# Kernel tuning notes

Measured on AMD Instinct MI355X. Metric: run time of the kernel, lower is better.

Reference implementation:

```python
import jax, jax.numpy as jnp
import numpy as np

B, N, C = 16, 3136, 384
H = W = 56
HEADS = 8
DH = C // HEADS
AG = 49          # agent_num
PS = 7           # pool size (sqrt(agent_num)); H % PS == 0 -> exact block mean
OUT = 1000
SCALE = DH ** -0.5


def setup_inputs() -> dict:
    key = jax.random.key(0)
    ks = jax.random.split(key, 16)
    f32 = jnp.float32

    def nrm(k, sh, s=0.02):
        return jax.random.normal(k, sh, f32) * s

    return dict(
        x=jax.random.normal(ks[0], (B, N, C), f32),
        Wq=nrm(ks[1], (C, C)),
        Wkv=nrm(ks[2], (C, 2 * C)),
        an_bias=nrm(ks[3], (HEADS, AG, H, W)),
        na_bias=nrm(ks[4], (HEADS, AG, H, W)),
        ah_bias=nrm(ks[5], (1, HEADS, AG, H, 1)),
        aw_bias=nrm(ks[6], (1, HEADS, AG, 1, W)),
        ha_bias=nrm(ks[7], (1, HEADS, H, 1, AG)),
        wa_bias=nrm(ks[8], (1, HEADS, 1, W, AG)),
        dwc_w=nrm(ks[9], (C, 1, 3, 3), 0.1),   # depthwise 3x3, groups=C (OIHW, I=1)
        dwc_b=jnp.zeros((C,), f32),
        Wproj=nrm(ks[10], (C, C)),
        bproj=jnp.zeros((C,), f32),
        ln_g=jnp.ones((C,), f32),
        ln_b=jnp.zeros((C,), f32),
        W1=nrm(ks[11], (C, 2 * C)),
        b1=jnp.zeros((2 * C,), f32),
        W2=nrm(ks[12], (2 * C, OUT)),
        b2=jnp.zeros((OUT,), f32),
    )


def _layernorm(x, g, b, eps=1e-5):
    m = x.mean(-1, keepdims=True)
    v = ((x - m) ** 2).mean(-1, keepdims=True)
    return (x - m) * jax.lax.rsqrt(v + eps) * g + b


def reference(x, Wq, Wkv, an_bias, na_bias, ah_bias, aw_bias, ha_bias, wa_bias,
              dwc_w, dwc_b, Wproj, bproj, ln_g, ln_b, W1, b1, W2, b2):
    q = x @ Wq                                  # (B,N,C)
    kv = x @ Wkv                                # (B,N,2C)  (sr_ratio=1 path)
    k, v = kv[..., :C], kv[..., C:]

    # agent tokens: AdaptiveAvgPool2d(7) on (B,C,56,56) == exact 8x8 block mean
    agent = q.reshape(B, PS, H // PS, PS, W // PS, C).mean((2, 4)).reshape(B, AG, C)

    qh = q.reshape(B, N, HEADS, DH).transpose(0, 2, 1, 3)      # (B,h,N,d)
    kh = k.reshape(B, N, HEADS, DH).transpose(0, 2, 1, 3)
    vh = v.reshape(B, N, HEADS, DH).transpose(0, 2, 1, 3)
    ah = agent.reshape(B, AG, HEADS, DH).transpose(0, 2, 1, 3)  # (B,h,AG,d)

    # stage 1: agent -> kv. bilinear interp to same size == identity (sr=1)
    pos_bias = an_bias.reshape(1, HEADS, AG, N) + (ah_bias + aw_bias).reshape(1, HEADS, AG, N)
    agent_attn = jax.nn.softmax(
        jnp.einsum('bhad,bhnd->bhan', ah * SCALE, kh) + pos_bias, axis=-1)
    agent_v = jnp.einsum('bhan,bhnd->bhad', agent_attn, vh)     # (B,h,AG,d)

    # stage 2: query -> agent
    agent_bias = (na_bias.reshape(1, HEADS, AG, N).transpose(0, 1, 3, 2)
                  + (ha_bias + wa_bias).reshape(1, HEADS, N, AG))
    q_attn = jax.nn.softmax(
        jnp.einsum('bhnd,bhad->bhna', qh * SCALE, ah) + agent_bias, axis=-1)
    out = jnp.einsum('bhna,bhad->bhnd', q_attn, agent_v)
    out = out.transpose(0, 2, 1, 3).reshape(B, N, C)

    # depthwise conv residual on v (sr=1 -> no interpolation)
    v_img = v.reshape(B, H, W, C).transpose(0, 3, 1, 2)          # (B,C,H,W)
    dwc = jax.lax.conv_general_dilated(
        v_img, dwc_w, (1, 1), 'SAME', feature_group_count=C,
        dimension_numbers=('NCHW', 'OIHW', 'NCHW')) + dwc_b[None, :, None, None]
    out = out + dwc.transpose(0, 2, 3, 1).reshape(B, N, C)

    out = out @ Wproj + bproj
    pooled = out.mean(axis=1)                   # adaptive_avg_pool2d to 1x1
    h1 = _layernorm(pooled, ln_g, ln_b)
    h1 = jax.nn.gelu(h1 @ W1 + b1, approximate=False)
    return h1 @ W2 + b2                         # (B, OUT)
```

## Files before the change

### kernel.cpp

```cpp
#include <hip/hip_runtime.h>
#include <hip/hip_bf16.h>
#include <math.h>

#define BB 16
#define NN 3136
#define CC 384
#define HDS 8
#define DHH 48
#define AGG 49
#define HI 56
#define WI 56
#define OUTD 1000
#define SCALE_F 0.14433756729740643f
#define QKVC 1152

typedef __attribute__((ext_vector_type(8))) short short8;
typedef __attribute__((ext_vector_type(4))) float f32x4;

__device__ __forceinline__ float bf2f(unsigned short u) {
  union { unsigned u32; float f; } x;
  x.u32 = ((unsigned)u) << 16;
  return x.f;
}
__device__ __forceinline__ unsigned short f2bf(float f) {
  union { float f; unsigned u; } x;
  x.f = f;
  unsigned u = x.u;
  unsigned r = (u + 0x7fffu + ((u >> 16) & 1u)) >> 16;
  return (unsigned short)r;
}

__device__ __forceinline__ size_t xp_off(int gb, int ks, int j, int lane) {
  return ((((size_t)gb * 12 + ks) * 4 + j) * 64 + lane) * 8;
}
__device__ __forceinline__ size_t wp_off(int blk, int ks, int i, int lane) {
  return ((((size_t)blk * 12 + ks) * 4 + i) * 64 + lane) * 8;
}
__device__ __forceinline__ size_t vtp_off(int bh, int chunk, int half, int ntd, int lane) {
  return ((((size_t)bh * 49 + chunk) * 2 + half) * 3 + ntd) * 512 + lane * 8;
}

__global__ __launch_bounds__(256) void pack_x(const float* __restrict__ x,
                                              unsigned short* __restrict__ xp) {
  __shared__ unsigned short xlds[64 * 200];
  int gb = blockIdx.x;
  int tid = threadIdx.x;
  int lane = tid & 63, wv = tid >> 6;
  int lo = lane & 15, g = lane >> 4;
  int tok0 = gb * 64;

  for (int kh = 0; kh < 2; kh++) {
    if (kh) __syncthreads();
#pragma unroll
    for (int it = 0; it < 12; it++) {
      int idx = tid + it * 256;
      int tok = idx / 48, k4 = idx % 48;
      float4 f = *(const float4*)&x[(size_t)(tok0 + tok) * 384 + kh * 192 + k4 * 4];
      uint2 o;
      o.x = (unsigned)f2bf(f.x) | ((unsigned)f2bf(f.y) << 16);
      o.y = (unsigned)f2bf(f.z) | ((unsigned)f2bf(f.w) << 16);
      *(uint2*)&xlds[tok * 200 + k4 * 4] = o;
    }
    __syncthreads();
    for (int p = wv; p < 24; p += 4) {
      int ks = p >> 2, j = p & 3;
      uint4 v = *(const uint4*)&xlds[(j * 16 + lo) * 200 + ks * 32 + g * 8];
      *(uint4*)&xp[xp_off(gb, kh * 6 + ks, j, lane)] = v;
    }
  }
}

__global__ __launch_bounds__(256) void pack_w(const float* __restrict__ Wq,
                                              const float* __restrict__ Wkv,
                                              unsigned short* __restrict__ wp) {
  __shared__ unsigned short wlds[64 * 392];
  int blk = blockIdx.x;
  int col0 = blk * 64;
  const float* src;
  int ncol, nloc;
  if (col0 < 384) { src = Wq; ncol = 384; nloc = col0; }
  else            { src = Wkv; ncol = 768; nloc = col0 - 384; }
  int tid = threadIdx.x;
  int lane = tid & 63, wv = tid >> 6;
  int lo = lane & 15, g = lane >> 4;

#pragma unroll
  for (int it = 0; it < 96; it++) {
    int idx = tid + it * 256;
    int k = idx >> 6, col = idx & 63;
    wlds[col * 392 + k] = f2bf(src[(size_t)k * ncol + nloc + col]);
  }
  __syncthreads();
  for (int p = wv; p < 48; p += 4) {
    int ks = p >> 2, i = p & 3;
    uint4 v = *(const uint4*)&wlds[(i * 16 + lo) * 392 + ks * 32 + g * 8];
    *(uint4*)&wp[wp_off(blk, ks, i, lane)] = v;
  }
}

__global__ __launch_bounds__(256, 2) void gemm_v4(const unsigned short* __restrict__ xp,
// ... 40 lines not shown
  auto mfmaF = [&](short8* wf, short8* xf) {
    __builtin_amdgcn_s_setprio(1);
#pragma unroll
    for (int i = 0; i < 4; i++)
#pragma unroll
      for (int jj = 0; jj < 8; jj++)
        acc[i][jj] = __builtin_amdgcn_mfma_f32_16x16x32_bf16(wf[i], xf[jj], acc[i][jj], 0, 0, 0);
    __builtin_amdgcn_s_setprio(0);
  };

  loadF(wfA, xfA, 0);
#pragma unroll
  for (int kp = 0; kp < 6; kp++) {
    loadF(wfB, xfB, 2 * kp + 1);
    mfmaF(wfA, xfA);
    if (kp < 5) loadF(wfA, xfA, 2 * kp + 2);
    mfmaF(wfB, xfB);
  }

#pragma unroll
  for (int jj = 0; jj < 8; jj++) {
    int token = (gbb + (jj >> 2)) * 64 + (jj & 3) * 16 + lo;
#pragma unroll
    for (int i = 0; i < 4; i++) {
      int ncol = bx * 128 + wn2 * 64 + i * 16 + g * 4;
      uint2 o;
      o.x = (unsigned)f2bf(acc[i][jj][0]) | ((unsigned)f2bf(acc[i][jj][1]) << 16);
      o.y = (unsigned)f2bf(acc[i][jj][2]) | ((unsigned)f2bf(acc[i][jj][3]) << 16);
      *(uint2*)&Y[(size_t)token * QKVC + ncol] = o;
    }
  }
}

__global__ __launch_bounds__(256) void make_cbias2(
    const float* __restrict__ na, const float* __restrict__ ha,
    const float* __restrict__ wa, const float* __restrict__ an,
    const float* __restrict__ ah, const float* __restrict__ aw,
    unsigned short* __restrict__ cb1t, unsigned short* __restrict__ cb2t) {
  int blk = blockIdx.x;
  int h = blk / 49, nc = blk % 49;
  int a = threadIdx.x & 63, sub = threadIdx.x >> 6;
  int ac = a < AGG ? a : AGG - 1;
  bool va = a < AGG;
  size_t hab = (size_t)h * AGG + ac;
#pragma unroll
  for (int i = 0; i < 16; i++) {
    int n = nc * 64 + i * 4 + sub;
    int r = n / WI, c = n % WI;
    float v1 = na[hab * NN + n] + ha[(h * HI + r) * AGG + ac] + wa[(h * WI + c) * AGG + ac];
    float v2 = an[hab * NN + n] + ah[hab * HI + r] + aw[hab * WI + c];
    size_t ob = ((size_t)h * NN + n) * 52;
    if (a < 52) {
      cb1t[ob + a] = va ? f2bf(v1) : (unsigned short)0;
      cb2t[ob + a] = va ? f2bf(v2) : (unsigned short)0;
    }
  }
}

#define VSTR 396
__global__ __launch_bounds__(256) void pack_vt(const unsigned short* __restrict__ qkv,
                                               unsigned short* __restrict__ vtp) {
  __shared__ unsigned short vlds[64 * VSTR];
  int blk = blockIdx.x;
  int b = blk / 49, chunk = blk % 49;
  int tid = threadIdx.x, lane = tid & 63, wv = tid >> 6;
  int lo = lane & 15, g = lane >> 4;

#pragma unroll
  for (int it = 0; it < 12; it++) {
    int idx = tid + it * 256;
    int t = idx / 48, d8 = idx % 48;
    short8 v = *(const short8*)&qkv[((size_t)b * NN + chunk * 64 + t) * QKVC + 768 + d8 * 8];
    *(uint2*)&vlds[t * VSTR + d8 * 8] = ((uint2*)&v)[0];
    *(uint2*)&vlds[t * VSTR + d8 * 8 + 4] = ((uint2*)&v)[1];
  }
  __syncthreads();
  int bh8 = b * 8;
#pragma unroll
  for (int p = 0; p < 12; p++) {
    int fid = wv * 12 + p;
    int h = fid / 6, rem = fid % 6, half = rem / 3, ntd = rem % 3;
    unsigned short tmp[8];
#pragma unroll
    for (int e = 0; e < 8; e++)
      tmp[e] = vlds[(half * 32 + g * 8 + e) * VSTR + h * 48 + ntd * 16 + lo];
    *(uint4*)&vtp[vtp_off(bh8 + h, chunk, half, ntd, lane)] = *(uint4*)tmp;
  }
}

__global__ __launch_bounds__(384) void pool_agent(const unsigned short* __restrict__ qkv,
                                                  unsigned short* __restrict__ agbf) {
  int blk = blockIdx.x;
  int b = blk / AGG, a = blk % AGG;
  int p1 = a / 7, p2 = a % 7;
  int c = threadIdx.x;
  float s = 0.f;
#pragma unroll
  for (int i = 0; i < 8; i++)
#pragma unroll
    for (int j = 0; j < 8; j++) {
      int n = (p1 * 8 + i) * WI + (p2 * 8 + j);
      s += bf2f(qkv[((size_t)b * NN + n) * QKVC + c]);
    }
  agbf[(size_t)blk * CC + c] = f2bf(s * (1.f / 64.f));
}

__global__ __launch_bounds__(256) void agent_attn_v5(
    const unsigned short* __restrict__ qkv, const unsigned short* __restrict__ agbf,
    const unsigned short* __restrict__ cb2t, const unsigned short* __restrict__ vtp,
    float* __restrict__ lpart, float* __restrict__ avpart) {
  int z = blockIdx.x;
  int s = z & 3;
  int h = (z >> 2) & 7;
  int b = z >> 5;
  int tid = threadIdx.x, lane = tid & 63, wv = tid >> 6;
  int lo = lane & 15, g = lane >> 4;
  int slot = s * 4 + wv;
  int cstart = (slot == 0) ? 0 : 3 * slot + 1;
  int ccount = (slot == 0) ? 4 : 3;
  int bh = b * 8 + h;

  __shared__ __align__(16) unsigned short pT[4][64 * 72];
  __shared__ float ldsAV[AGG * 48];
  __shared__ float ldsL[AGG];
  for (int i = tid; i < AGG * 48; i += 256) ldsAV[i] = 0.f;
  if (tid < AGG) ldsL[tid] = 0.f;
  __syncthreads();

  short8 af0[4], af1[4];
#pragma unroll
  for (int mt = 0; mt < 4; mt++) {
    int a = mt * 16 + lo;
    int ac = a < AGG ? a : AGG - 1;
    const unsigned short* p = agbf + ((size_t)b * AGG + ac) * CC + h * 48;
    af0[mt] = *(const short8*)(p + g * 8);
    if (g < 2) af1[mt] = *(const short8*)(p + 32 + g * 8);
    else { short8 zz = {0, 0, 0, 0, 0, 0, 0, 0}; af1[mt] = zz; }
  }

  f32x4 acc2[4][3];
#pragma unroll
  for (int mt = 0; mt < 4; mt++)
#pragma unroll
    for (int ntd = 0; ntd < 3; ntd++) acc2[mt][ntd] = (f32x4)0.f;
  float lacc[4][4];
#pragma unroll
  for (int mt = 0; mt < 4; mt++)
#pragma unroll
    for (int r = 0; r < 4; r++) lacc[mt][r] = 0.f;

  for (int ci = 0; ci < ccount; ci++) {
    int chunk = cstart + ci;
    int nb = chunk * 64;

    short8 kf0[4], kf1[4];
#pragma unroll
    for (int nt = 0; nt < 4; nt++) {
      const unsigned short* kp = qkv + ((size_t)b * NN + nb + nt * 16 + lo) * QKVC + 384 + h * 48;
      kf0[nt] = *(const short8*)(kp + g * 8);
      if (g < 2) kf1[nt] = *(const short8*)(kp + 32 + g * 8);
      else { short8 zz = {0, 0, 0, 0, 0, 0, 0, 0}; kf1[nt] = zz; }
    }
    ushort4 cbv[4][4];
#pragma unroll
    for (int mt = 0; mt < 4; mt++)
#pragma unroll
      for (int nt = 0; nt < 4; nt++)
        cbv[mt][nt] = *(const ushort4*)&cb2t[((size_t)h * NN + nb + nt * 16 + lo) * 52 + mt * 16 + g * 4];
    short8 vb0[3], vb1[3];
#pragma unroll
    for (int ntd = 0; ntd < 3; ntd++) {
      vb0[ntd] = *(const short8*)&vtp[vtp_off(bh, chunk, 0, ntd, lane)];
      vb1[ntd] = *(const short8*)&vtp[vtp_off(bh, chunk, 1, ntd, lane)];
    }

    f32x4 acc[4][4];
#pragma unroll
    for (int mt = 0; mt < 4; mt++)
#pragma unroll
      for (int nt = 0; nt < 4; nt++) acc[mt][nt] = (f32x4)0.f;
#pragma unroll
    for (int mt = 0; mt < 4; mt++)
#pragma unroll
      for (int nt = 0; nt < 4; nt++) {
        acc[mt][nt] = __builtin_amdgcn_mfma_f32_16x16x32_bf16(af0[mt], kf0[nt], acc[mt][nt], 0, 0, 0);
        acc[mt][nt] = __builtin_amdgcn_mfma_f32_16x16x32_bf16(af1[mt], kf1[nt], acc[mt][nt], 0, 0, 0);
      }

#pragma unroll
    for (int mt = 0; mt < 4; mt++)
#pragma unroll
      for (int nt = 0; nt < 4; nt++) {
        unsigned short cb4[4] = {cbv[mt][nt].x, cbv[mt][nt].y, cbv[mt][nt].z, cbv[mt][nt].w};
#pragma unroll
        for (int r = 0; r < 4; r++) {
          int a = mt * 16 + g * 4 + r;
          float e = 0.f;
          if (a < AGG) e = __expf(acc[mt][nt][r] * SCALE_F + bf2f(cb4[r]));
          acc[mt][nt][r] = e;
        }
      }
#pragma unroll
    for (int mt = 0; mt < 4; mt++)
#pragma unroll
      for (int r = 0; r < 4; r++)
        lacc[mt][r] += acc[mt][0][r] + acc[mt][1][r] + acc[mt][2][r] + acc[mt][3][r];
#pragma unroll
    for (int mt = 0; mt < 4; mt++)
#pragma unroll
      for (int nt = 0; nt < 4; nt++)
#pragma unroll
        for (int r = 0; r < 4; r++) {
          int a = mt * 16 + g * 4 + r;
          int t = nt * 16 + lo;
          pT[wv][a * 72 + t] = f2bf(acc[mt][nt][r]);
        }

    short8 pa0[4], pa1[4];
#pragma unroll
    for (int mt = 0; mt < 4; mt++) {
      const unsigned short* p = &pT[wv][(mt * 16 + lo) * 72 + g * 8];
      pa0[mt] = *(const short8*)p;
      pa1[mt] = *(const short8*)(p + 32);
    }
#pragma unroll
    for (int mt = 0; mt < 4; mt++)
#pragma unroll
      for (int ntd = 0; ntd < 3; ntd++) {
        acc2[mt][ntd] = __builtin_amdgcn_mfma_f32_16x16x32_bf16(pa0[mt], vb0[ntd], acc2[mt][ntd], 0, 0, 0);
        acc2[mt][ntd] = __builtin_amdgcn_mfma_f32_16x16x32_bf16(pa1[mt], vb1[ntd], acc2[mt][ntd], 0, 0, 0);
      }
  }

#pragma unroll
  for (int mt = 0; mt < 4; mt++)
#pragma unroll
    for (int r = 0; r < 4; r++) {
      float v = lacc[mt][r];
      v += __shfl_xor(v, 1); v += __shfl_xor(v, 2);
      v += __shfl_xor(v, 4); v += __shfl_xor(v, 8);
      if (lo == 0) {
        int a = mt * 16 + g * 4 + r;
        if (a < AGG) atomicAdd(&ldsL[a], v);
      }
    }
#pragma unroll
  for (int mt = 0; mt < 4; mt++)
#pragma unroll
    for (int ntd = 0; ntd < 3; ntd++)
#pragma unroll
      for (int r = 0; r < 4; r++) {
        int a = mt * 16 + g * 4 + r;
        if (a < AGG) atomicAdd(&ldsAV[a * 48 + ntd * 16 + lo], acc2[mt][ntd][r]);
      }
  __syncthreads();
  size_t pbase = (size_t)bh * 4 + s;
  for (int i = tid; i < AGG * 48; i += 256) avpart[pbase * 2352 + i] = ldsAV[i];
  if (tid < AGG) lpart[pbase * AGG + tid] = ldsL[tid];
}

__global__ __launch_bounds__(256) void av_normalize4(const float* __restrict__ lpart,
                                                     const float* __restrict__ avpart,
                                                     float* __restrict__ av) {
  int bh = blockIdx.x;
  int tid = threadIdx.x;
  __shared__ float linv[AGG];
  if (tid < AGG) {
    float l = 0.f;
#pragma unroll
    for (int s = 0; s < 4; s++) l += lpart[((size_t)bh * 4 + s) * AGG + tid];
    linv[tid] = 1.f / l;
  }
  __syncthreads();
  for (int idx = tid; idx < AGG * 48; idx += 256) {
    int a = idx / 48;
    float v = 0.f;
#pragma unroll
    for (int s = 0; s < 4; s++) v += avpart[((size_t)bh * 4 + s) * 2352 + idx];
    av[(size_t)bh * 2352 + idx] = v * linv[a];
  }
}

__global__ __launch_bounds__(256) void q_attn_v9(
    const unsigned short* __restrict__ qkv, const unsigned short* __restrict__ agbf,
    const unsigned short* __restrict__ cb1t, float* __restrict__ opart) {
  int z = blockIdx.x;
  int s = z & 3;
  int h = (z >> 2) & 7;
  int b = z >> 5;
  int tid = threadIdx.x, lane = tid & 63, wv = tid >> 6;
  int lo = lane & 15, g = lane >> 4;
  int slot = s * 4 + wv;
  int cstart = (slot == 0) ? 0 : 3 * slot + 1;
  int ccount = (slot == 0) ? 4 : 3;
  int bh = b * 8 + h;

  short8 af0[4], af1[4];
#pragma unroll
  for (int mt = 0; mt < 4; mt++) {
    int a = mt * 16 + lo;
    int ac = a < AGG ? a : AGG - 1;
    const unsigned short* p = agbf + ((size_t)b * AGG + ac) * CC + h * 48;
    af0[mt] = *(const short8*)(p + g * 8);
    if (g < 2) af1[mt] = *(const short8*)(p + 32 + g * 8);
    else { short8 zz = {0, 0, 0, 0, 0, 0, 0, 0}; af1[mt] = zz; }
  }

  float psum[4][4];
#pragma unroll
  for (int mt = 0; mt < 4; mt++)
#pragma unroll
    for (int r = 0; r < 4; r++) psum[mt][r] = 0.f;

  for (int ci = 0; ci < ccount; ci++) {
    int nb = (cstart + ci) * 64;

    short8 qf0[4], qf1[4];
#pragma unroll
    for (int nt = 0; nt < 4; nt++) {
      const unsigned short* qp = qkv + ((size_t)b * NN + nb + nt * 16 + lo) * QKVC + h * 48;
      qf0[nt] = *(const short8*)(qp + g * 8);
      if (g < 2) qf1[nt] = *(const short8*)(qp + 32 + g * 8);
      else { short8 zz = {0, 0, 0, 0, 0, 0, 0, 0}; qf1[nt] = zz; }
    }
    ushort4 cbv[4][4];
#pragma unroll
    for (int mt = 0; mt < 4; mt++)
#pragma unroll
      for (int nt = 0; nt < 4; nt++)
        cbv[mt][nt] = *(const ushort4*)&cb1t[((size_t)h * NN + nb + nt * 16 + lo) * 52 + mt * 16 + g * 4];

    f32x4 acc[4][4];
#pragma unroll
    for (int mt = 0; mt < 4; mt++)
#pragma unroll
      for (int nt = 0; nt < 4; nt++) acc[mt][nt] = (f32x4)0.f;
#pragma unroll
    for (int mt = 0; mt < 4; mt++)
#pragma unroll
      for (int nt = 0; nt < 4; nt++) {
        acc[mt][nt] = __builtin_amdgcn_mfma_f32_16x16x32_bf16(af0[mt], qf0[nt], acc[mt][nt], 0, 0, 0);
        acc[mt][nt] = __builtin_amdgcn_mfma_f32_16x16x32_bf16(af1[mt], qf1[nt], acc[mt][nt], 0, 0, 0);
      }

#pragma unroll
    for (int nt = 0; nt < 4; nt++) {
      float lsum = 0.f;
#pragma unroll
      for (int mt = 0; mt < 4; mt++) {
        unsigned short cb4[4] = {cbv[mt][nt].x, cbv[mt][nt].y, cbv[mt][nt].z, cbv[mt][nt].w};
#pragma unroll
        for (int r = 0; r < 4; r++) {
          int a = mt * 16 + g * 4 + r;
          float e = 0.f;
          if (a < AGG) e = __expf(acc[mt][nt][r] * SCALE_F + bf2f(cb4[r]));
          acc[mt][nt][r] = e;
          lsum += e;
        }
      }
      lsum += __shfl_xor(lsum, 16);
      lsum += __shfl_xor(lsum, 32);
      float inv = 1.f / lsum;
#pragma unroll
      for (int mt = 0; mt < 4; mt++)
#pragma unroll
        for (int r = 0; r < 4; r++)
          psum[mt][r] += acc[mt][nt][r] * inv;
    }
  }

  size_t pbase = (size_t)bh * 16 + slot;
#pragma unroll
  for (int mt = 0; mt < 4; mt++)
#pragma unroll
    for (int r = 0; r < 4; r++) {
      float v = psum[mt][r];
      v += __shfl_xor(v, 1); v += __shfl_xor(v, 2);
      v += __shfl_xor(v, 4); v += __shfl_xor(v, 8);
      int a = mt * 16 + g * 4 + r;
      if (lo == 0 && a < AGG) opart[pbase * 52 + a] = v;
    }
}

__global__ __launch_bounds__(384) void dwc_rows(const unsigned short* __restrict__ qkv,
                                                float* __restrict__ rowsum,
                                                float* __restrict__ edge0,
                                                float* __restrict__ edge1) {
  int z = blockIdx.x;
  int b = z / HI, r = z % HI;
  int c = threadIdx.x;
  const unsigned short* base = qkv + ((size_t)b * NN + (size_t)r * WI) * QKVC + 768 + c;
  float s = 0.f, e0 = 0.f, e1 = 0.f;
  for (int w = 0; w < WI; w++) {
    float v = bf2f(base[(size_t)w * QKVC]);
    s += v;
    if (w == 0) e0 = v;
    if (w == WI - 1) e1 = v;
  }
  rowsum[(size_t)z * CC + c] = s;
  edge0[(size_t)z * CC + c] = e0;
  edge1[(size_t)z * CC + c] = e1;
}

__global__ __launch_bounds__(384) void dwc_combine1(const float* __restrict__ rowsum,
                                                    const float* __restrict__ edge0,
                                                    const float* __restrict__ edge1,
                                                    float* __restrict__ dpart,
                                                    float* __restrict__ dedge) {
  int z = blockIdx.x;
  int b = z / 7, rc = z % 7;
  int c = threadIdx.x;
  float T = 0.f, C0 = 0.f, C55 = 0.f;
#pragma unroll
  for (int rr = 0; rr < 8; rr++) {
    int r = rc * 8 + rr;
    size_t idx = ((size_t)(b * HI + r)) * CC + c;
    float rs = rowsum[idx], a0 = edge0[idx], a1 = edge1[idx];
    T += rs; C0 += a0; C55 += a1;
    if (r == 0) {
      dedge[((size_t)b * 6 + 0) * CC + c] = rs;
      dedge[((size_t)b * 6 + 1) * CC + c] = a0;
      dedge[((size_t)b * 6 + 2) * CC + c] = a1;
    }
    if (r == HI - 1) {
      dedge[((size_t)b * 6 + 3) * CC + c] = rs;
      dedge[((size_t)b * 6 + 4) * CC + c] = a0;
      dedge[((size_t)b * 6 + 5) * CC + c] = a1;
    }
  }
  size_t pb = ((size_t)(b * 7 + rc) * 3) * CC + c;
  dpart[pb] = T;
  dpart[pb + CC] = C0;
  dpart[pb + 2 * CC] = C55;
}
// ... 196 lines not shown
  const float* W1 = (const float*)d_in[15];
  const float* b1 = (const float*)d_in[16];
  const float* W2 = (const float*)d_in[17];
  const float* b2 = (const float*)d_in[18];
  float* out = (float*)d_out;

  const size_t M = (size_t)BB * NN;
  char* wsp = (char*)d_ws;
  unsigned short* xp = (unsigned short*)wsp;
  unsigned short* vtp = xp;
  wsp += M * CC * 2;
  unsigned short* wpb = (unsigned short*)wsp;   wsp += (size_t)QKVC * CC * 2;
  unsigned short* qkv = (unsigned short*)wsp;   wsp += M * QKVC * 2;
  unsigned short* agbf = (unsigned short*)wsp;  wsp += (size_t)784 * CC * 2;
  unsigned short* cb1t = (unsigned short*)wsp;  wsp += (size_t)HDS * NN * 52 * 2;
  unsigned short* cb2t = (unsigned short*)wsp;  wsp += (size_t)HDS * NN * 52 * 2;
  float* lpart = (float*)wsp;                   wsp += (size_t)128 * 4 * AGG * 4;
  float* avpart = (float*)wsp;                  wsp += (size_t)128 * 4 * 2352 * 4;
  float* av = (float*)wsp;                      wsp += (size_t)128 * 2352 * 4;
  float* opart = (float*)wsp;                   wsp += (size_t)128 * 16 * 52 * 4;
  float* rowsum = (float*)wsp;                  wsp += (size_t)BB * HI * CC * 4;
  float* edge0 = (float*)wsp;                   wsp += (size_t)BB * HI * CC * 4;
  float* edge1 = (float*)wsp;                   wsp += (size_t)BB * HI * CC * 4;
  float* dpart = (float*)wsp;                   wsp += (size_t)BB * 7 * 3 * CC * 4;
  float* dedge = (float*)wsp;                   wsp += (size_t)BB * 6 * CC * 4;
  float* pre = (float*)wsp;                     wsp += (size_t)BB * CC * 4;
  float* pjpart = (float*)wsp;                  wsp += (size_t)BB * 6 * CC * 4;
  float* h0b = (float*)wsp;                     wsp += (size_t)BB * CC * 4;
  float* h1part = (float*)wsp;                  wsp += (size_t)BB * 6 * 2 * CC * 4;
  float* h1b = (float*)wsp;                     wsp += (size_t)BB * 2 * CC * 4;
  float* o2part = (float*)wsp;                  wsp += (size_t)BB * 12 * 1024 * 4;

  dim3 blk256(256);
  hipLaunchKernelGGL(pack_x, dim3(784), blk256, 0, stream, x, xp);
  hipLaunchKernelGGL(pack_w, dim3(18), blk256, 0, stream, Wq, Wkv, wpb);
  hipLaunchKernelGGL(make_cbias2, dim3(HDS * 49), blk256, 0, stream, na_bias,
                     ha_bias, wa_bias, an_bias, ah_bias, aw_bias, cb1t, cb2t);
  hipLaunchKernelGGL(gemm_v4, dim3(1764), blk256, 0, stream, xp, wpb, qkv);
  hipLaunchKernelGGL(pack_vt, dim3(BB * 49), blk256, 0, stream, qkv, vtp);
  hipLaunchKernelGGL(pool_agent, dim3(BB * AGG), dim3(384), 0, stream, qkv, agbf);
  hipLaunchKernelGGL(agent_attn_v5, dim3(BB * HDS * 4), blk256, 0, stream,
                     qkv, agbf, cb2t, vtp, lpart, avpart);
  hipLaunchKernelGGL(av_normalize4, dim3(BB * HDS), blk256, 0, stream, lpart,
                     avpart, av);
  hipLaunchKernelGGL(q_attn_v9, dim3(BB * HDS * 4), blk256, 0, stream, qkv,
                     agbf, cb1t, opart);
  hipLaunchKernelGGL(dwc_rows, dim3(BB * HI), dim3(384), 0, stream, qkv, rowsum,
                     edge0, edge1);
  hipLaunchKernelGGL(dwc_combine1, dim3(BB * 7), dim3(384), 0, stream, rowsum,
                     edge0, edge1, dpart, dedge);
  hipLaunchKernelGGL(head_pre, dim3(BB), dim3(384), 0, stream, dpart, dedge,
                     opart, av, dwc_w, dwc_b, pre);
  hipLaunchKernelGGL(head_proj_part, dim3(144), blk256, 0, stream, pre, Wproj, pjpart);
  hipLaunchKernelGGL(head_ln6, dim3(BB), dim3(384), 0, stream, pjpart, bproj,
                     ln_g, ln_b, h0b);
  hipLaunchKernelGGL(head_mlp1_part, dim3(288), blk256, 0, stream, h0b, W1, h1part);
  hipLaunchKernelGGL(head_mlp1_red, dim3(BB), blk256, 0, stream, h1part, b1, h1b);
  hipLaunchKernelGGL(head_mlp2_part, dim3(768), blk256, 0, stream, h1b, W2, o2part);
  hipLaunchKernelGGL(head_out, dim3(BB), blk256, 0, stream, o2part, b2, out);
}
```

Measured before the change: 265.8 us.

## Merge independent kernels into block-indexed fused launches to cut launch count

Combines independent kernels into shared launches that branch on block index. pack_x runs with make_cbias2, pack_vt with pool_agent, and agent attention with query attention and the dwc row sums. This removes several launch gaps and lets independent work fill the GPU together. In exchange, the fused kernels share the largest LDS footprint and register pressure of their branches, which may lower occupancy for the lighter blocks. pool_agent and dwc_rows now run at 256 threads looping over channels instead of 384.

```diff
diff --git a/kernel.cpp b/kernel.cpp
--- a/kernel.cpp
+++ b/kernel.cpp
@@ -40,32 +40,57 @@
   return ((((size_t)bh * 49 + chunk) * 2 + half) * 3 + ntd) * 512 + lane * 8;
 }
 
-__global__ __launch_bounds__(256) void pack_x(const float* __restrict__ x,
-                                              unsigned short* __restrict__ xp) {
+__global__ __launch_bounds__(256) void pack_x_cbias(
+    const float* __restrict__ x, unsigned short* __restrict__ xp,
+    const float* __restrict__ na, const float* __restrict__ ha,
+    const float* __restrict__ wa, const float* __restrict__ an,
+    const float* __restrict__ ah, const float* __restrict__ aw,
+    unsigned short* __restrict__ cb1t, unsigned short* __restrict__ cb2t) {
   __shared__ unsigned short xlds[64 * 200];
-  int gb = blockIdx.x;
+  int z = blockIdx.x;
   int tid = threadIdx.x;
-  int lane = tid & 63, wv = tid >> 6;
-  int lo = lane & 15, g = lane >> 4;
-  int tok0 = gb * 64;
-
-  for (int kh = 0; kh < 2; kh++) {
-    if (kh) __syncthreads();
-#pragma unroll
-    for (int it = 0; it < 12; it++) {
-      int idx = tid + it * 256;
-      int tok = idx / 48, k4 = idx % 48;
-      float4 f = *(const float4*)&x[(size_t)(tok0 + tok) * 384 + kh * 192 + k4 * 4];
-      uint2 o;
-      o.x = (unsigned)f2bf(f.x) | ((unsigned)f2bf(f.y) << 16);
-      o.y = (unsigned)f2bf(f.z) | ((unsigned)f2bf(f.w) << 16);
-      *(uint2*)&xlds[tok * 200 + k4 * 4] = o;
-    }
-    __syncthreads();
-    for (int p = wv; p < 24; p += 4) {
-      int ks = p >> 2, j = p & 3;
-      uint4 v = *(const uint4*)&xlds[(j * 16 + lo) * 200 + ks * 32 + g * 8];
-      *(uint4*)&xp[xp_off(gb, kh * 6 + ks, j, lane)] = v;
+  if (z < 784) {
+    int gb = z;
+    int lane = tid & 63, wv = tid >> 6;
+    int lo = lane & 15, g = lane >> 4;
+    int tok0 = gb * 64;
+    for (int kh = 0; kh < 2; kh++) {
+      if (kh) __syncthreads();
+#pragma unroll
+      for (int it = 0; it < 12; it++) {
+        int idx = tid + it * 256;
+        int tok = idx / 48, k4 = idx % 48;
+        float4 f = *(const float4*)&x[(size_t)(tok0 + tok) * 384 + kh * 192 + k4 * 4];
+        uint2 o;
+        o.x = (unsigned)f2bf(f.x) | ((unsigned)f2bf(f.y) << 16);
+        o.y = (unsigned)f2bf(f.z) | ((unsigned)f2bf(f.w) << 16);
+        *(uint2*)&xlds[tok * 200 + k4 * 4] = o;
+      }
+      __syncthreads();
+      for (int p = wv; p < 24; p += 4) {
+        int ks = p >> 2, j = p & 3;
+        uint4 v = *(const uint4*)&xlds[(j * 16 + lo) * 200 + ks * 32 + g * 8];
+        *(uint4*)&xp[xp_off(gb, kh * 6 + ks, j, lane)] = v;
+      }
+    }
+  } else {
+    int blk = z - 784;
+    int h = blk / 49, nc = blk % 49;
+    int a = tid & 63, sub = tid >> 6;
+    int ac = a < AGG ? a : AGG - 1;
+    bool va = a < AGG;
+    size_t hab = (size_t)h * AGG + ac;
+#pragma unroll
+    for (int i = 0; i < 16; i++) {
+      int n = nc * 64 + i * 4 + sub;
+      int r = n / WI, c = n % WI;
+      float v1 = na[hab * NN + n] + ha[(h * HI + r) * AGG + ac] + wa[(h * WI + c) * AGG + ac];
+      float v2 = an[hab * NN + n] + ah[hab * HI + r] + aw[hab * WI + c];
+      size_t ob = ((size_t)h * NN + n) * 52;
+      if (a < 52) {
+        cb1t[ob + a] = va ? f2bf(v1) : (unsigned short)0;
+        cb2t[ob + a] = va ? f2bf(v2) : (unsigned short)0;
+      }
     }
   }
 }
@@ -172,231 +197,327 @@
   }
 }
 
-__global__ __launch_bounds__(256) void make_cbias2(
-    const float* __restrict__ na, const float* __restrict__ ha,
-    const float* __restrict__ wa, const float* __restrict__ an,
-    const float* __restrict__ ah, const float* __restrict__ aw,
-    unsigned short* __restrict__ cb1t, unsigned short* __restrict__ cb2t) {
-  int blk = blockIdx.x;
-  int h = blk / 49, nc = blk % 49;
-  int a = threadIdx.x & 63, sub = threadIdx.x >> 6;
-  int ac = a < AGG ? a : AGG - 1;
-  bool va = a < AGG;
-  size_t hab = (size_t)h * AGG + ac;
-#pragma unroll
-  for (int i = 0; i < 16; i++) {
-    int n = nc * 64 + i * 4 + sub;
-    int r = n / WI, c = n % WI;
-    float v1 = na[hab * NN + n] + ha[(h * HI + r) * AGG + ac] + wa[(h * WI + c) * AGG + ac];
-    float v2 = an[hab * NN + n] + ah[hab * HI + r] + aw[hab * WI + c];
-    size_t ob = ((size_t)h * NN + n) * 52;
-    if (a < 52) {
-      cb1t[ob + a] = va ? f2bf(v1) : (unsigned short)0;
-      cb2t[ob + a] = va ? f2bf(v2) : (unsigned short)0;
-    }
-  }
-}
-
 #define VSTR 396
-__global__ __launch_bounds__(256) void pack_vt(const unsigned short* __restrict__ qkv,
-                                               unsigned short* __restrict__ vtp) {
+__global__ __launch_bounds__(256) void prep2_fused(const unsigned short* __restrict__ qkv,
+                                                   unsigned short* __restrict__ vtp,
+                                                   unsigned short* __restrict__ agbf) {
   __shared__ unsigned short vlds[64 * VSTR];
-  int blk = blockIdx.x;
-  int b = blk / 49, chunk = blk % 49;
-  int tid = threadIdx.x, lane = tid & 63, wv = tid >> 6;
-  int lo = lane & 15, g = lane >> 4;
-
-#pragma unroll
-  for (int it = 0; it < 12; it++) {
-    int idx = tid + it * 256;
-    int t = idx / 48, d8 = idx % 48;
-    short8 v = *(const short8*)&qkv[((size_t)b * NN + chunk * 64 + t) * QKVC + 768 + d8 * 8];
-    *(uint2*)&vlds[t * VSTR + d8 * 8] = ((uint2*)&v)[0];
-    *(uint2*)&vlds[t * VSTR + d8 * 8 + 4] = ((uint2*)&v)[1];
-  }
-  __syncthreads();
-  int bh8 = b * 8;
-#pragma unroll
-  for (int p = 0; p < 12; p++) {
-    int fid = wv * 12 + p;
-    int h = fid / 6, rem = fid % 6, half = rem / 3, ntd = rem % 3;
-    unsigned short tmp[8];
-#pragma unroll
-    for (int e = 0; e < 8; e++)
-      tmp[e] = vlds[(half * 32 + g * 8 + e) * VSTR + h * 48 + ntd * 16 + lo];
-    *(uint4*)&vtp[vtp_off(bh8 + h, chunk, half, ntd, lane)] = *(uint4*)tmp;
-  }
-}
-
-__global__ __launch_bounds__(384) void pool_agent(const unsigned short* __restrict__ qkv,
-                                                  unsigned short* __restrict__ agbf) {
-  int blk = blockIdx.x;
-  int b = blk / AGG, a = blk % AGG;
-  int p1 = a / 7, p2 = a % 7;
-  int c = threadIdx.x;
-  float s = 0.f;
-#pragma unroll
-  for (int i = 0; i < 8; i++)
-#pragma unroll
-    for (int j = 0; j < 8; j++) {
-      int n = (p1 * 8 + i) * WI + (p2 * 8 + j);
-      s += bf2f(qkv[((size_t)b * NN + n) * QKVC + c]);
-    }
-  agbf[(size_t)blk * CC + c] = f2bf(s * (1.f / 64.f));
-}
-
-__global__ __launch_bounds__(256) void agent_attn_v5(
+  int z = blockIdx.x;
+  int tid = threadIdx.x;
+  if (z < 784) {
+    int b = z / 49, chunk = z % 49;
+    int lane = tid & 63, wv = tid >> 6;
+    int lo = lane & 15, g = lane >> 4;
+#pragma unroll
+    for (int it = 0; it < 12; it++) {
+      int idx = tid + it * 256;
+      int t = idx / 48, d8 = idx % 48;
+      short8 v = *(const short8*)&qkv[((size_t)b * NN + chunk * 64 + t) * QKVC + 768 + d8 * 8];
+      *(uint2*)&vlds[t * VSTR + d8 * 8] = ((uint2*)&v)[0];
+      *(uint2*)&vlds[t * VSTR + d8 * 8 + 4] = ((uint2*)&v)[1];
+    }
+    __syncthreads();
+    int bh8 = b * 8;
+#pragma unroll
+    for (int p = 0; p < 12; p++) {
+      int fid = wv * 12 + p;
+      int h = fid / 6, rem = fid % 6, half = rem / 3, ntd = rem % 3;
+      unsigned short tmp[8];
+#pragma unroll
+      for (int e = 0; e < 8; e++)
+        tmp[e] = vlds[(half * 32 + g * 8 + e) * VSTR + h * 48 + ntd * 16 + lo];
+      *(uint4*)&vtp[vtp_off(bh8 + h, chunk, half, ntd, lane)] = *(uint4*)tmp;
+    }
+  } else {
+    int blk = z - 784;
+    int b = blk / AGG, a = blk % AGG;
+    int p1 = a / 7, p2 = a % 7;
+    for (int c = tid; c < CC; c += 256) {
+      float s = 0.f;
+#pragma unroll
+      for (int i = 0; i < 8; i++)
+#pragma unroll
+        for (int j = 0; j < 8; j++) {
+          int n = (p1 * 8 + i) * WI + (p2 * 8 + j);
+          s += bf2f(qkv[((size_t)b * NN + n) * QKVC + c]);
+        }
+      agbf[(size_t)blk * CC + c] = f2bf(s * (1.f / 64.f));
+    }
+  }
+}
+
+__global__ __launch_bounds__(256) void attn_dwc_fused(
     const unsigned short* __restrict__ qkv, const unsigned short* __restrict__ agbf,
-    const unsigned short* __restrict__ cb2t, const unsigned short* __restrict__ vtp,
-    float* __restrict__ lpart, float* __restrict__ avpart) {
-  int z = blockIdx.x;
-  int s = z & 3;
-  int h = (z >> 2) & 7;
-  int b = z >> 5;
-  int tid = threadIdx.x, lane = tid & 63, wv = tid >> 6;
-  int lo = lane & 15, g = lane >> 4;
-  int slot = s * 4 + wv;
-  int cstart = (slot == 0) ? 0 : 3 * slot + 1;
-  int ccount = (slot == 0) ? 4 : 3;
-  int bh = b * 8 + h;
-
+    const unsigned short* __restrict__ cb1t, const unsigned short* __restrict__ cb2t,
+    const unsigned short* __restrict__ vtp, float* __restrict__ lpart,
+    float* __restrict__ avpart, float* __restrict__ opart,
+    float* __restrict__ rowsum, float* __restrict__ edge0,
+    float* __restrict__ edge1) {
   __shared__ __align__(16) unsigned short pT[4][64 * 72];
   __shared__ float ldsAV[AGG * 48];
   __shared__ float ldsL[AGG];
-  for (int i = tid; i < AGG * 48; i += 256) ldsAV[i] = 0.f;
-  if (tid < AGG) ldsL[tid] = 0.f;
-  __syncthreads();
-
-  short8 af0[4], af1[4];
-#pragma unroll
-  for (int mt = 0; mt < 4; mt++) {
-    int a = mt * 16 + lo;
-    int ac = a < AGG ? a : AGG - 1;
-    const unsigned short* p = agbf + ((size_t)b * AGG + ac) * CC + h * 48;
-    af0[mt] = *(const short8*)(p + g * 8);
-    if (g < 2) af1[mt] = *(const short8*)(p + 32 + g * 8);
-    else { short8 zz = {0, 0, 0, 0, 0, 0, 0, 0}; af1[mt] = zz; }
-  }
-
-  f32x4 acc2[4][3];
-#pragma unroll
-  for (int mt = 0; mt < 4; mt++)
-#pragma unroll
-    for (int ntd = 0; ntd < 3; ntd++) acc2[mt][ntd] = (f32x4)0.f;
-  float lacc[4][4];
-#pragma unroll
-  for (int mt = 0; mt < 4; mt++)
-#pragma unroll
-    for (int r = 0; r < 4; r++) lacc[mt][r] = 0.f;
-
-  for (int ci = 0; ci < ccount; ci++) {
-    int chunk = cstart + ci;
-    int nb = chunk * 64;
-
-    short8 kf0[4], kf1[4];
-#pragma unroll
-    for (int nt = 0; nt < 4; nt++) {
-      const unsigned short* kp = qkv + ((size_t)b * NN + nb + nt * 16 + lo) * QKVC + 384 + h * 48;
-      kf0[nt] = *(const short8*)(kp + g * 8);
-      if (g < 2) kf1[nt] = *(const short8*)(kp + 32 + g * 8);
-      else { short8 zz = {0, 0, 0, 0, 0, 0, 0, 0}; kf1[nt] = zz; }
-    }
-    ushort4 cbv[4][4];
+
+  int z = blockIdx.x;
+  int tid = threadIdx.x, lane = tid & 63, wv = tid >> 6;
+  int lo = lane & 15, g = lane >> 4;
+
+  if (z < 512) {
+    int s = z & 3;
+    int h = (z >> 2) & 7;
+    int b = z >> 5;
+    int slot = s * 4 + wv;
+    int cstart = (slot == 0) ? 0 : 3 * slot + 1;
+    int ccount = (slot == 0) ? 4 : 3;
+    int bh = b * 8 + h;
+
+    for (int i = tid; i < AGG * 48; i += 256) ldsAV[i] = 0.f;
+    if (tid < AGG) ldsL[tid] = 0.f;
+    __syncthreads();
+
+    short8 af0[4], af1[4];
+#pragma unroll
+    for (int mt = 0; mt < 4; mt++) {
+      int a = mt * 16 + lo;
+      int ac = a < AGG ? a : AGG - 1;
+      const unsigned short* p = agbf + ((size_t)b * AGG + ac) * CC + h * 48;
+      af0[mt] = *(const short8*)(p + g * 8);
+      if (g < 2) af1[mt] = *(const short8*)(p + 32 + g * 8);
+      else { short8 zz = {0, 0, 0, 0, 0, 0, 0, 0}; af1[mt] = zz; }
+    }
+
+    f32x4 acc2[4][3];
 #pragma unroll
     for (int mt = 0; mt < 4; mt++)
 #pragma unroll
-      for (int nt = 0; nt < 4; nt++)
-        cbv[mt][nt] = *(const ushort4*)&cb2t[((size_t)h * NN + nb + nt * 16 + lo) * 52 + mt * 16 + g * 4];
-    short8 vb0[3], vb1[3];
-#pragma unroll
-    for (int ntd = 0; ntd < 3; ntd++) {
-      vb0[ntd] = *(const short8*)&vtp[vtp_off(bh, chunk, 0, ntd, lane)];
-      vb1[ntd] = *(const short8*)&vtp[vtp_off(bh, chunk, 1, ntd, lane)];
-    }
-
-    f32x4 acc[4][4];
+      for (int ntd = 0; ntd < 3; ntd++) acc2[mt][ntd] = (f32x4)0.f;
+    float lacc[4][4];
 #pragma unroll
     for (int mt = 0; mt < 4; mt++)
 #pragma unroll
-      for (int nt = 0; nt < 4; nt++) acc[mt][nt] = (f32x4)0.f;
+      for (int r = 0; r < 4; r++) lacc[mt][r] = 0.f;
+
+    for (int ci = 0; ci < ccount; ci++) {
+      int chunk = cstart + ci;
+      int nb = chunk * 64;
+
+      short8 kf0[4], kf1[4];
+#pragma unroll
+      for (int nt = 0; nt < 4; nt++) {
+        const unsigned short* kp = qkv + ((size_t)b * NN + nb + nt * 16 + lo) * QKVC + 384 + h * 48;
+        kf0[nt] = *(const short8*)(kp + g * 8);
+        if (g < 2) kf1[nt] = *(const short8*)(kp + 32 + g * 8);
+        else { short8 zz = {0, 0, 0, 0, 0, 0, 0, 0}; kf1[nt] = zz; }
+      }
+      ushort4 cbv[4][4];
+#pragma unroll
+      for (int mt = 0; mt < 4; mt++)
+#pragma unroll
+        for (int nt = 0; nt < 4; nt++)
+          cbv[mt][nt] = *(const ushort4*)&cb2t[((size_t)h * NN + nb + nt * 16 + lo) * 52 + mt * 16 + g * 4];
+      short8 vb0[3], vb1[3];
+#pragma unroll
+      for (int ntd = 0; ntd < 3; ntd++) {
+        vb0[ntd] = *(const short8*)&vtp[vtp_off(bh, chunk, 0, ntd, lane)];
+        vb1[ntd] = *(const short8*)&vtp[vtp_off(bh, chunk, 1, ntd, lane)];
+      }
+
+      f32x4 acc[4][4];
+#pragma unroll
+      for (int mt = 0; mt < 4; mt++)
+#pragma unroll
+        for (int nt = 0; nt < 4; nt++) acc[mt][nt] = (f32x4)0.f;
+#pragma unroll
+      for (int mt = 0; mt < 4; mt++)
+#pragma unroll
+        for (int nt = 0; nt < 4; nt++) {
+          acc[mt][nt] = __builtin_amdgcn_mfma_f32_16x16x32_bf16(af0[mt], kf0[nt], acc[mt][nt], 0, 0, 0);
+          acc[mt][nt] = __builtin_amdgcn_mfma_f32_16x16x32_bf16(af1[mt], kf1[nt], acc[mt][nt], 0, 0, 0);
+        }
+
+#pragma unroll
+      for (int mt = 0; mt < 4; mt++)
+#pragma unroll
+        for (int nt = 0; nt < 4; nt++) {
+          unsigned short cb4[4] = {cbv[mt][nt].x, cbv[mt][nt].y, cbv[mt][nt].z, cbv[mt][nt].w};
+#pragma unroll
+          for (int r = 0; r < 4; r++) {
+            int a = mt * 16 + g * 4 + r;
+            float e = 0.f;
+            if (a < AGG) e = __expf(acc[mt][nt][r] * SCALE_F + bf2f(cb4[r]));
+            acc[mt][nt][r] = e;
+          }
+        }
+#pragma unroll
+      for (int mt = 0; mt < 4; mt++)
+#pragma unroll
+        for (int r = 0; r < 4; r++)
+          lacc[mt][r] += acc[mt][0][r] + acc[mt][1][r] + acc[mt][2][r] + acc[mt][3][r];
+#pragma unroll
+      for (int mt = 0; mt < 4; mt++)
+#pragma unroll
+        for (int nt = 0; nt < 4; nt++)
+#pragma unroll
+          for (int r = 0; r < 4; r++) {
+            int a = mt * 16 + g * 4 + r;
+            int t = nt * 16 + lo;
+            pT[wv][a * 72 + t] = f2bf(acc[mt][nt][r]);
+          }
+
+      short8 pa0[4], pa1[4];
+#pragma unroll
+      for (int mt = 0; mt < 4; mt++) {
+        const unsigned short* p = &pT[wv][(mt * 16 + lo) * 72 + g * 8];
+        pa0[mt] = *(const short8*)p;
+        pa1[mt] = *(const short8*)(p + 32);
+      }
+#pragma unroll
+      for (int mt = 0; mt < 4; mt++)
+#pragma unroll
+        for (int ntd = 0; ntd < 3; ntd++) {
+          acc2[mt][ntd] = __builtin_amdgcn_mfma_f32_16x16x32_bf16(pa0[mt], vb0[ntd], acc2[mt][ntd], 0, 0, 0);
+          acc2[mt][ntd] = __builtin_amdgcn_mfma_f32_16x16x32_bf16(pa1[mt], vb1[ntd], acc2[mt][ntd], 0, 0, 0);
+        }
+    }
+
 #pragma unroll
     for (int mt = 0; mt < 4; mt++)
 #pragma unroll
-      for (int nt = 0; nt < 4; nt++) {
-        acc[mt][nt] = __builtin_amdgcn_mfma_f32_16x16x32_bf16(af0[mt], kf0[nt], acc[mt][nt], 0, 0, 0);
-        acc[mt][nt] = __builtin_amdgcn_mfma_f32_16x16x32_bf16(af1[mt], kf1[nt], acc[mt][nt], 0, 0, 0);
-      }
-
+      for (int r = 0; r < 4; r++) {
+        float v = lacc[mt][r];
+        v += __shfl_xor(v, 1); v += __shfl_xor(v, 2);
+        v += __shfl_xor(v, 4); v += __shfl_xor(v, 8);
+        if (lo == 0) {
+          int a = mt * 16 + g * 4 + r;
+          if (a < AGG) atomicAdd(&ldsL[a], v);
+        }
+      }
 #pragma unroll
     for (int mt = 0; mt < 4; mt++)
 #pragma unroll
-      for (int nt = 0; nt < 4; nt++) {
-        unsigned short cb4[4] = {cbv[mt][nt].x, cbv[mt][nt].y, cbv[mt][nt].z, cbv[mt][nt].w};
+      for (int ntd = 0; ntd < 3; ntd++)
 #pragma unroll
         for (int r = 0; r < 4; r++) {
           int a = mt * 16 + g * 4 + r;
-          float e = 0.f;
-          if (a < AGG) e = __expf(acc[mt][nt][r] * SCALE_F + bf2f(cb4[r]));
-          acc[mt][nt][r] = e;
+          if (a < AGG) atomicAdd(&ldsAV[a * 48 + ntd * 16 + lo], acc2[mt][ntd][r]);
         }
-      }
+    __syncthreads();
+    size_t pbase = (size_t)bh * 4 + s;
+    for (int i = tid; i < AGG * 48; i += 256) avpart[pbase * 2352 + i] = ldsAV[i];
+    if (tid < AGG) lpart[pbase * AGG + tid] = ldsL[tid];
+
+  } else if (z < 1024) {
+    int zz = z - 512;
+    int s = zz & 3;
+    int h = (zz >> 2) & 7;
+    int b = zz >> 5;
+    int slot = s * 4 + wv;
+    int cstart = (slot == 0) ? 0 : 3 * slot + 1;
+    int ccount = (slot == 0) ? 4 : 3;
+    int bh = b * 8 + h;
+
+    short8 af0[4], af1[4];
+#pragma unroll
+    for (int mt = 0; mt < 4; mt++) {
+      int a = mt * 16 + lo;
+      int ac = a < AGG ? a : AGG - 1;
+      const unsigned short* p = agbf + ((size_t)b * AGG + ac) * CC + h * 48;
+      af0[mt] = *(const short8*)(p + g * 8);
+      if (g < 2) af1[mt] = *(const short8*)(p + 32 + g * 8);
+      else { short8 zz2 = {0, 0, 0, 0, 0, 0, 0, 0}; af1[mt] = zz2; }
+    }
+
+    float psum[4][4];
 #pragma unroll
     for (int mt = 0; mt < 4; mt++)
 #pragma unroll
-      for (int r = 0; r < 4; r++)
-        lacc[mt][r] += acc[mt][0][r] + acc[mt][1][r] + acc[mt][2][r] + acc[mt][3][r];
+      for (int r = 0; r < 4; r++) psum[mt][r] = 0.f;
+
+    for (int ci = 0; ci < ccount; ci++) {
+      int nb = (cstart + ci) * 64;
+
+      short8 qf0[4], qf1[4];
+#pragma unroll
+      for (int nt = 0; nt < 4; nt++) {
+        const unsigned short* qp = qkv + ((size_t)b * NN + nb + nt * 16 + lo) * QKVC + h * 48;
+        qf0[nt] = *(const short8*)(qp + g * 8);
+        if (g < 2) qf1[nt] = *(const short8*)(qp + 32 + g * 8);
+        else { short8 zz2 = {0, 0, 0, 0, 0, 0, 0, 0}; qf1[nt] = zz2; }
+      }
+      ushort4 cbv[4][4];
+#pragma unroll
+      for (int mt = 0; mt < 4; mt++)
+#pragma unroll
+        for (int nt = 0; nt < 4; nt++)
+          cbv[mt][nt] = *(const ushort4*)&cb1t[((size_t)h * NN + nb + nt * 16 + lo) * 52 + mt * 16 + g * 4];
+
+      f32x4 acc[4][4];
+#pragma unroll
+      for (int mt = 0; mt < 4; mt++)
+#pragma unroll
+        for (int nt = 0; nt < 4; nt++) acc[mt][nt] = (f32x4)0.f;
+#pragma unroll
+      for (int mt = 0; mt < 4; mt++)
+#pragma unroll
+        for (int nt = 0; nt < 4; nt++) {
+          acc[mt][nt] = __builtin_amdgcn_mfma_f32_16x16x32_bf16(af0[mt], qf0[nt], acc[mt][nt], 0, 0, 0);
+          acc[mt][nt] = __builtin_amdgcn_mfma_f32_16x16x32_bf16(af1[mt], qf1[nt], acc[mt][nt], 0, 0, 0);
+        }
+
+#pragma unroll
+      for (int nt = 0; nt < 4; nt++) {
+        float lsum = 0.f;
+#pragma unroll
+        for (int mt = 0; mt < 4; mt++) {
+          unsigned short cb4[4] = {cbv[mt][nt].x, cbv[mt][nt].y, cbv[mt][nt].z, cbv[mt][nt].w};
+#pragma unroll
+          for (int r = 0; r < 4; r++) {
+            int a = mt * 16 + g * 4 + r;
+            float e = 0.f;
+            if (a < AGG) e = __expf(acc[mt][nt][r] * SCALE_F + bf2f(cb4[r]));
+            acc[mt][nt][r] = e;
+            lsum += e;
+          }
+        }
+        lsum += __shfl_xor(lsum, 16);
+        lsum += __shfl_xor(lsum, 32);
+        float inv = 1.f / lsum;
+#pragma unroll
+        for (int mt = 0; mt < 4; mt++)
+#pragma unroll
+          for (int r = 0; r < 4; r++)
+            psum[mt][r] += acc[mt][nt][r] * inv;
+      }
+    }
+
+    size_t pbase = (size_t)bh * 16 + slot;
 #pragma unroll
     for (int mt = 0; mt < 4; mt++)
 #pragma unroll
-      for (int nt = 0; nt < 4; nt++)
-#pragma unroll
-        for (int r = 0; r < 4; r++) {
-          int a = mt * 16 + g * 4 + r;
-          int t = nt * 16 + lo;
-          pT[wv][a * 72 + t] = f2bf(acc[mt][nt][r]);
-        }
-
-    short8 pa0[4], pa1[4];
-#pragma unroll
-    for (int mt = 0; mt < 4; mt++) {
-      const unsigned short* p = &pT[wv][(mt * 16 + lo) * 72 + g * 8];
-      pa0[mt] = *(const short8*)p;
-      pa1[mt] = *(const short8*)(p + 32);
-    }
-#pragma unroll
-    for (int mt = 0; mt < 4; mt++)
-#pragma unroll
-      for (int ntd = 0; ntd < 3; ntd++) {
-        acc2[mt][ntd] = __builtin_amdgcn_mfma_f32_16x16x32_bf16(pa0[mt], vb0[ntd], acc2[mt][ntd], 0, 0, 0);
-        acc2[mt][ntd] = __builtin_amdgcn_mfma_f32_16x16x32_bf16(pa1[mt], vb1[ntd], acc2[mt][ntd], 0, 0, 0);
-      }
-  }
-
-#pragma unroll
-  for (int mt = 0; mt < 4; mt++)
-#pragma unroll
-    for (int r = 0; r < 4; r++) {
-      float v = lacc[mt][r];
-      v += __shfl_xor(v, 1); v += __shfl_xor(v, 2);
-      v += __shfl_xor(v, 4); v += __shfl_xor(v, 8);
-      if (lo == 0) {
+      for (int r = 0; r < 4; r++) {
+        float v = psum[mt][r];
+        v += __shfl_xor(v, 1); v += __shfl_xor(v, 2);
+        v += __shfl_xor(v, 4); v += __shfl_xor(v, 8);
         int a = mt * 16 + g * 4 + r;
-        if (a < AGG) atomicAdd(&ldsL[a], v);
-      }
-    }
-#pragma unroll
-  for (int mt = 0; mt < 4; mt++)
-#pragma unroll
-    for (int ntd = 0; ntd < 3; ntd++)
-#pragma unroll
-      for (int r = 0; r < 4; r++) {
-        int a = mt * 16 + g * 4 + r;
-        if (a < AGG) atomicAdd(&ldsAV[a * 48 + ntd * 16 + lo], acc2[mt][ntd][r]);
-      }
-  __syncthreads();
-  size_t pbase = (size_t)bh * 4 + s;
-  for (int i = tid; i < AGG * 48; i += 256) avpart[pbase * 2352 + i] = ldsAV[i];
-  if (tid < AGG) lpart[pbase * AGG + tid] = ldsL[tid];
+        if (lo == 0 && a < AGG) opart[pbase * 52 + a] = v;
+      }
+
+  } else {
+    int zz = z - 1024;
+    int b = zz / HI, r = zz % HI;
+    for (int c = tid; c < CC; c += 256) {
+      const unsigned short* base = qkv + ((size_t)b * NN + (size_t)r * WI) * QKVC + 768 + c;
+      float sum = 0.f, e0v = 0.f, e1v = 0.f;
+      for (int w = 0; w < WI; w++) {
+        float v = bf2f(base[(size_t)w * QKVC]);
+        sum += v;
+        if (w == 0) e0v = v;
+        if (w == WI - 1) e1v = v;
+      }
+      rowsum[(size_t)zz * CC + c] = sum;
+      edge0[(size_t)zz * CC + c] = e0v;
+      edge1[(size_t)zz * CC + c] = e1v;
+    }
+  }
 }
 
 __global__ __launch_bounds__(256) void av_normalize4(const float* __restrict__ lpart,
@@ -419,127 +540,6 @@
     for (int s = 0; s < 4; s++) v += avpart[((size_t)bh * 4 + s) * 2352 + idx];
     av[(size_t)bh * 2352 + idx] = v * linv[a];
   }
-}
-
-__global__ __launch_bounds__(256) void q_attn_v9(
-    const unsigned short* __restrict__ qkv, const unsigned short* __restrict__ agbf,
-    const unsigned short* __restrict__ cb1t, float* __restrict__ opart) {
-  int z = blockIdx.x;
-  int s = z & 3;
-  int h = (z >> 2) & 7;
-  int b = z >> 5;
-  int tid = threadIdx.x, lane = tid & 63, wv = tid >> 6;
-  int lo = lane & 15, g = lane >> 4;
-  int slot = s * 4 + wv;
-  int cstart = (slot == 0) ? 0 : 3 * slot + 1;
-  int ccount = (slot == 0) ? 4 : 3;
-  int bh = b * 8 + h;
-
-  short8 af0[4], af1[4];
-#pragma unroll
-  for (int mt = 0; mt < 4; mt++) {
-    int a = mt * 16 + lo;
-    int ac = a < AGG ? a : AGG - 1;
-    const unsigned short* p = agbf + ((size_t)b * AGG + ac) * CC + h * 48;
-    af0[mt] = *(const short8*)(p + g * 8);
-    if (g < 2) af1[mt] = *(const short8*)(p + 32 + g * 8);
-    else { short8 zz = {0, 0, 0, 0, 0, 0, 0, 0}; af1[mt] = zz; }
-  }
-
-  float psum[4][4];
-#pragma unroll
-  for (int mt = 0; mt < 4; mt++)
-#pragma unroll
-    for (int r = 0; r < 4; r++) psum[mt][r] = 0.f;
-
-  for (int ci = 0; ci < ccount; ci++) {
-    int nb = (cstart + ci) * 64;
-
-    short8 qf0[4], qf1[4];
-#pragma unroll
-    for (int nt = 0; nt < 4; nt++) {
-      const unsigned short* qp = qkv + ((size_t)b * NN + nb + nt * 16 + lo) * QKVC + h * 48;
-      qf0[nt] = *(const short8*)(qp + g * 8);
-      if (g < 2) qf1[nt] = *(const short8*)(qp + 32 + g * 8);
-      else { short8 zz = {0, 0, 0, 0, 0, 0, 0, 0}; qf1[nt] = zz; }
-    }
-    ushort4 cbv[4][4];
-#pragma unroll
-    for (int mt = 0; mt < 4; mt++)
-#pragma unroll
-      for (int nt = 0; nt < 4; nt++)
-        cbv[mt][nt] = *(const ushort4*)&cb1t[((size_t)h * NN + nb + nt * 16 + lo) * 52 + mt * 16 + g * 4];
-
-    f32x4 acc[4][4];
-#pragma unroll
-    for (int mt = 0; mt < 4; mt++)
-#pragma unroll
-      for (int nt = 0; nt < 4; nt++) acc[mt][nt] = (f32x4)0.f;
-#pragma unroll
-    for (int mt = 0; mt < 4; mt++)
-#pragma unroll
-      for (int nt = 0; nt < 4; nt++) {
-        acc[mt][nt] = __builtin_amdgcn_mfma_f32_16x16x32_bf16(af0[mt], qf0[nt], acc[mt][nt], 0, 0, 0);
-        acc[mt][nt] = __builtin_amdgcn_mfma_f32_16x16x32_bf16(af1[mt], qf1[nt], acc[mt][nt], 0, 0, 0);
-      }
-
-#pragma unroll
-    for (int nt = 0; nt < 4; nt++) {
-      float lsum = 0.f;
-#pragma unroll
-      for (int mt = 0; mt < 4; mt++) {
-        unsigned short cb4[4] = {cbv[mt][nt].x, cbv[mt][nt].y, cbv[mt][nt].z, cbv[mt][nt].w};
-#pragma unroll
-        for (int r = 0; r < 4; r++) {
-          int a = mt * 16 + g * 4 + r;
-          float e = 0.f;
-          if (a < AGG) e = __expf(acc[mt][nt][r] * SCALE_F + bf2f(cb4[r]));
-          acc[mt][nt][r] = e;
-          lsum += e;
-        }
-      }
-      lsum += __shfl_xor(lsum, 16);
-      lsum += __shfl_xor(lsum, 32);
-      float inv = 1.f / lsum;
-#pragma unroll
-      for (int mt = 0; mt < 4; mt++)
-#pragma unroll
-        for (int r = 0; r < 4; r++)
-          psum[mt][r] += acc[mt][nt][r] * inv;
-    }
-  }
-
-  size_t pbase = (size_t)bh * 16 + slot;
-#pragma unroll
-  for (int mt = 0; mt < 4; mt++)
-#pragma unroll
-    for (int r = 0; r < 4; r++) {
-      float v = psum[mt][r];
-      v += __shfl_xor(v, 1); v += __shfl_xor(v, 2);
-      v += __shfl_xor(v, 4); v += __shfl_xor(v, 8);
-      int a = mt * 16 + g * 4 + r;
-      if (lo == 0 && a < AGG) opart[pbase * 52 + a] = v;
-    }
-}
-
-__global__ __launch_bounds__(384) void dwc_rows(const unsigned short* __restrict__ qkv,
-                                                float* __restrict__ rowsum,
-                                                float* __restrict__ edge0,
-                                                float* __restrict__ edge1) {
-  int z = blockIdx.x;
-  int b = z / HI, r = z % HI;
-  int c = threadIdx.x;
-  const unsigned short* base = qkv + ((size_t)b * NN + (size_t)r * WI) * QKVC + 768 + c;
-  float s = 0.f, e0 = 0.f, e1 = 0.f;
-  for (int w = 0; w < WI; w++) {
-    float v = bf2f(base[(size_t)w * QKVC]);
-    s += v;
-    if (w == 0) e0 = v;
-    if (w == WI - 1) e1 = v;
-  }
-  rowsum[(size_t)z * CC + c] = s;
-  edge0[(size_t)z * CC + c] = e0;
-  edge1[(size_t)z * CC + c] = e1;
 }
 
 __global__ __launch_bounds__(384) void dwc_combine1(const float* __restrict__ rowsum,
@@ -802,21 +802,16 @@
   float* o2part = (float*)wsp;                  wsp += (size_t)BB * 12 * 1024 * 4;
 
   dim3 blk256(256);
-  hipLaunchKernelGGL(pack_x, dim3(784), blk256, 0, stream, x, xp);
+  hipLaunchKernelGGL(pack_x_cbias, dim3(1176), blk256, 0, stream, x, xp,
+                     na_bias, ha_bias, wa_bias, an_bias, ah_bias, aw_bias,
+                     cb1t, cb2t);
   hipLaunchKernelGGL(pack_w, dim3(18), blk256, 0, stream, Wq, Wkv, wpb);
-  hipLaunchKernelGGL(make_cbias2, dim3(HDS * 49), blk256, 0, stream, na_bias,
-                     ha_bias, wa_bias, an_bias, ah_bias, aw_bias, cb1t, cb2t);
   hipLaunchKernelGGL(gemm_v4, dim3(1764), blk256, 0, stream, xp, wpb, qkv);
-  hipLaunchKernelGGL(pack_vt, dim3(BB * 49), blk256, 0, stream, qkv, vtp);
-  hipLaunchKernelGGL(pool_agent, dim3(BB * AGG), dim3(384), 0, stream, qkv, agbf);
-  hipLaunchKernelGGL(agent_attn_v5, dim3(BB * HDS * 4), blk256, 0, stream,
-                     qkv, agbf, cb2t, vtp, lpart, avpart);
+  hipLaunchKernelGGL(prep2_fused, dim3(1568), blk256, 0, stream, qkv, vtp, agbf);
+  hipLaunchKernelGGL(attn_dwc_fused, dim3(1920), blk256, 0, stream, qkv, agbf,
+                     cb1t, cb2t, vtp, lpart, avpart, opart, rowsum, edge0, edge1);
   hipLaunchKernelGGL(av_normalize4, dim3(BB * HDS), blk256, 0, stream, lpart,
                      avpart, av);
-  hipLaunchKernelGGL(q_attn_v9, dim3(BB * HDS * 4), blk256, 0, stream, qkv,
-                     agbf, cb1t, opart);
-  hipLaunchKernelGGL(dwc_rows, dim3(BB * HI), dim3(384), 0, stream, qkv, rowsum,
-                     edge0, edge1);
   hipLaunchKernelGGL(dwc_combine1, dim3(BB * 7), dim3(384), 0, stream, rowsum,
                      edge0, edge1, dpart, dedge);
   hipLaunchKernelGGL(head_pre, dim3(BB), dim3(384), 0, stream, dpart, dedge,
```

Result: slower. 271.9 us (+2.3%).
